# Performance work log

Measured on AMD Instinct MI355X. Metric: run time of the kernel, lower is better.

## Reference

```python
import jax, jax.numpy as jnp
import numpy as np

SCALING = 2.0  # alpha / rank = 16 / 8


def _kron(A, B):
    # A: (m, n), B: (p, q) -> (m*p, n*q), same broadcast-multiply-reshape as torch code
    m, n = A.shape
    p, q = B.shape
    return (A[:, None, :, None] * B[None, :, None, :]).reshape(m * p, n * q)


def setup_inputs() -> dict:
    key = jax.random.key(0)
    k1, k2, k3, k4 = jax.random.split(key, 4)
    x = jax.random.normal(k1, (128, 8192), dtype=jnp.float32)
    original_weight = jax.random.normal(k2, (8192, 8192), dtype=jnp.float32) * 0.02
    lokr_A = jax.random.normal(k3, (512, 8192), dtype=jnp.float32) * 0.02
    lokr_B = jax.random.normal(k4, (16, 1), dtype=jnp.float32) * 0.02
    scalar = jnp.ones((1,), dtype=jnp.float32)
    return {"x": x, "original_weight": original_weight, "lokr_A": lokr_A,
            "lokr_B": lokr_B, "scalar": scalar}


def reference(x, original_weight, lokr_A, lokr_B, scalar):
    # delta_W = (A kron B) * scaling ; W_eff = W + scalar * delta_W ; out = x @ W_eff^T
    delta_W = _kron(lokr_A, lokr_B) * SCALING          # (8192, 8192)
    W_eff = original_weight + scalar[0] * delta_W      # bypass_mode with original weight
    return x @ W_eff.T                                 # dropout=0 -> identity
```

## Files before the change

### kernel.cpp

```cpp
#include <hip/hip_runtime.h>


#define M_DIM 128
#define N_DIM 8192
#define K_DIM 8192
#define BN 32
#define NWAVE 8
#define KW (K_DIM / NWAVE)

typedef __attribute__((ext_vector_type(8))) short bf16x8;
typedef __attribute__((ext_vector_type(4))) float f32x4;

__device__ __forceinline__ unsigned short f2bf(float f) {
  unsigned u = __builtin_bit_cast(unsigned, f);
  u += 0x7FFFu + ((u >> 16) & 1u);
  return (unsigned short)(u >> 16);
}

__device__ __forceinline__ bf16x8 cvt8(float4 a, float4 b) {
  bf16x8 r;
  r[0] = (short)f2bf(a.x); r[1] = (short)f2bf(a.y);
  r[2] = (short)f2bf(a.z); r[3] = (short)f2bf(a.w);
  r[4] = (short)f2bf(b.x); r[5] = (short)f2bf(b.y);
  r[6] = (short)f2bf(b.z); r[7] = (short)f2bf(b.w);
  return r;
}

__global__ void convert_x_kernel(const float4* __restrict__ x4,
                                 ushort4* __restrict__ xb4) {
  int t = blockIdx.x * blockDim.x + threadIdx.x;
  const int n4 = M_DIM * K_DIM / 4;
  for (int i = t; i < n4; i += gridDim.x * blockDim.x) {
    float4 v = x4[i];
    ushort4 o;
    o.x = f2bf(v.x); o.y = f2bf(v.y); o.z = f2bf(v.z); o.w = f2bf(v.w);
    xb4[i] = o;
  }
}

__global__ __launch_bounds__(512, 2) void lokr_main(
    const float* __restrict__ W,
    const float* __restrict__ A,
    const float* __restrict__ Bv,
    const float* __restrict__ scal,
    const unsigned short* __restrict__ xb,
    float* __restrict__ out)
{
  __shared__ float red[NWAVE * M_DIM * 16];

  const int t    = threadIdx.x;
  const int lane = t & 63;
  const int wv   = t >> 6;
  const int b    = blockIdx.x;
  const int l15  = lane & 15;
  const int l4   = lane >> 4;
  const int kw   = wv * KW;

  const float sB = 2.0f * scal[0] * Bv[l15];

  f32x4 accW[8][2];
  f32x4 accY[8];
  const f32x4 z4 = {0.f, 0.f, 0.f, 0.f};
#pragma unroll
  for (int mf = 0; mf < 8; ++mf) {
    accY[mf] = z4;
    accW[mf][0] = z4;
    accW[mf][1] = z4;
  }

  const float* Wp = W + (size_t)(b * BN + l15) * K_DIM + kw + l4 * 8;
  const float* Ap = A + (size_t)(2 * b + (l15 >> 3)) * K_DIM + kw + l4 * 8;
  const unsigned short* xp = xb + (size_t)l15 * K_DIM + kw + l4 * 8;

  float4 wr[2][2][2];
  float4 ar[2][2];
#pragma unroll
  for (int nf = 0; nf < 2; ++nf)
#pragma unroll
    for (int kk = 0; kk < 2; ++kk)
#pragma unroll
      for (int h = 0; h < 2; ++h)
        wr[nf][kk][h] = *(const float4*)(Wp + (size_t)nf * 16 * K_DIM + kk * 32 + h * 4);
#pragma unroll
  for (int kk = 0; kk < 2; ++kk)
#pragma unroll
    for (int h = 0; h < 2; ++h)
      ar[kk][h] = *(const float4*)(Ap + kk * 32 + h * 4);

  for (int kt = 0; kt < KW; kt += 64) {
    bf16x8 wbf[2][2], abf[2];
#pragma unroll
    for (int nf = 0; nf < 2; ++nf)
#pragma unroll
      for (int kk = 0; kk < 2; ++kk)
        wbf[nf][kk] = cvt8(wr[nf][kk][0], wr[nf][kk][1]);
#pragma unroll
    for (int kk = 0; kk < 2; ++kk)
      abf[kk] = cvt8(ar[kk][0], ar[kk][1]);

    if (kt + 64 < KW) {
#pragma unroll
      for (int nf = 0; nf < 2; ++nf)
#pragma unroll
        for (int kk = 0; kk < 2; ++kk)
#pragma unroll
          for (int h = 0; h < 2; ++h)
            wr[nf][kk][h] = *(const float4*)(Wp + (size_t)nf * 16 * K_DIM + kt + 64 + kk * 32 + h * 4);
#pragma unroll
      for (int kk = 0; kk < 2; ++kk)
#pragma unroll
        for (int h = 0; h < 2; ++h)
          ar[kk][h] = *(const float4*)(Ap + kt + 64 + kk * 32 + h * 4);
    }

#pragma unroll
    for (int kk = 0; kk < 2; ++kk) {
      bf16x8 xa[8];
#pragma unroll
      for (int mf = 0; mf < 8; ++mf)
        xa[mf] = *(const bf16x8*)(xp + (size_t)mf * 16 * K_DIM + kt + kk * 32);
#pragma unroll
      for (int mf = 0; mf < 8; ++mf) {
        accW[mf][0] = __builtin_amdgcn_mfma_f32_16x16x32_bf16(xa[mf], wbf[0][kk], accW[mf][0], 0, 0, 0);
        accW[mf][1] = __builtin_amdgcn_mfma_f32_16x16x32_bf16(xa[mf], wbf[1][kk], accW[mf][1], 0, 0, 0);
        accY[mf]    = __builtin_amdgcn_mfma_f32_16x16x32_bf16(xa[mf], abf[kk],    accY[mf],    0, 0, 0);
      }
    }
  }

#pragma unroll 1
  for (int nf = 0; nf < 2; ++nf) {
    if (nf) __syncthreads();
#pragma unroll
    for (int mf = 0; mf < 8; ++mf) {
#pragma unroll
      for (int r = 0; r < 4; ++r) {
        float y2v = __shfl(accY[mf][r], (lane & 48) | (nf << 3), 64);
        int m = mf * 16 + l4 * 4 + r;
        red[wv * 2048 + m * 16 + l15] = accW[mf][nf][r] + sB * y2v;
      }
    }
    __syncthreads();
    const float* rp = red + t * 4;
    float4 s = *(const float4*)rp;
#pragma unroll
    for (int w = 1; w < NWAVE; ++w) {
      float4 v = *(const float4*)(rp + w * 2048);
      s.x += v.x; s.y += v.y; s.z += v.z; s.w += v.w;
    }
    int m  = t >> 2;
    int c0 = (t & 3) * 4;
    *(float4*)(out + (size_t)m * N_DIM + b * BN + nf * 16 + c0) = s;
  }
}

extern "C" void kernel_launch(void* const* d_in, const int* in_sizes, int n_in,
                              void* d_out, int out_size, void* d_ws, size_t ws_size,
                              hipStream_t stream) {
  const float* x    = (const float*)d_in[0];
  const float* W    = (const float*)d_in[1];
  const float* A    = (const float*)d_in[2];
  const float* Bv   = (const float*)d_in[3];
  const float* scal = (const float*)d_in[4];
  float* out = (float*)d_out;

  unsigned short* xb = (unsigned short*)d_ws;

  convert_x_kernel<<<512, 256, 0, stream>>>((const float4*)x, (ushort4*)xb);
  lokr_main<<<N_DIM / BN, 512, 0, stream>>>(W, A, Bv, scal, xb, out);
}
```

Baseline: 454.5 us.

## Split waves across M and K halves with double-buffered W and x loads

Reorganizes the 8 waves into 2 M-groups by 4 K-slices, so each wave computes 64 rows over a 2048-wide K range with half the accumulators. Adds explicit ping-pong register buffering of W, A and the bf16 x fragments to overlap global loads with MFMA work. This reduces register pressure and x-load volume per wave, but each W/A element is now loaded and converted by two waves, increasing cache traffic and conversion ALU work.

```diff
diff --git a/kernel.cpp b/kernel.cpp
--- a/kernel.cpp
+++ b/kernel.cpp
@@ -5,8 +5,7 @@
 #define N_DIM 8192
 #define K_DIM 8192
 #define BN 32
-#define NWAVE 8
-#define KW (K_DIM / NWAVE)
+#define KWC (K_DIM / 4)
 
 typedef __attribute__((ext_vector_type(8))) short bf16x8;
 typedef __attribute__((ext_vector_type(4))) float f32x4;
@@ -38,6 +37,37 @@
   }
 }
 
+#define LOADW(koff, w, a) { \
+    w[0] = *(const float4*)(Wp + (koff)); \
+    w[1] = *(const float4*)(Wp + (koff) + 4); \
+    w[2] = *(const float4*)(Wp + 16 * (size_t)K_DIM + (koff)); \
+    w[3] = *(const float4*)(Wp + 16 * (size_t)K_DIM + (koff) + 4); \
+    a[0] = *(const float4*)(Ap + (koff)); \
+    a[1] = *(const float4*)(Ap + (koff) + 4); \
+  }
+
+#define LOADX(koff, x) { \
+    x[0] = *(const bf16x8*)(xp + (koff)); \
+    x[1] = *(const bf16x8*)(xp + 16 * (size_t)K_DIM + (koff)); \
+    x[2] = *(const bf16x8*)(xp + 32 * (size_t)K_DIM + (koff)); \
+    x[3] = *(const bf16x8*)(xp + 48 * (size_t)K_DIM + (koff)); \
+  }
+
+#define MFMA_STEP(x, w0, w1, ab) { \
+    accW[0][0] = __builtin_amdgcn_mfma_f32_16x16x32_bf16(x[0], w0, accW[0][0], 0, 0, 0); \
+    accW[0][1] = __builtin_amdgcn_mfma_f32_16x16x32_bf16(x[0], w1, accW[0][1], 0, 0, 0); \
+    accY[0]    = __builtin_amdgcn_mfma_f32_16x16x32_bf16(x[0], ab, accY[0],    0, 0, 0); \
+    accW[1][0] = __builtin_amdgcn_mfma_f32_16x16x32_bf16(x[1], w0, accW[1][0], 0, 0, 0); \
+    accW[1][1] = __builtin_amdgcn_mfma_f32_16x16x32_bf16(x[1], w1, accW[1][1], 0, 0, 0); \
+    accY[1]    = __builtin_amdgcn_mfma_f32_16x16x32_bf16(x[1], ab, accY[1],    0, 0, 0); \
+    accW[2][0] = __builtin_amdgcn_mfma_f32_16x16x32_bf16(x[2], w0, accW[2][0], 0, 0, 0); \
+    accW[2][1] = __builtin_amdgcn_mfma_f32_16x16x32_bf16(x[2], w1, accW[2][1], 0, 0, 0); \
+    accY[2]    = __builtin_amdgcn_mfma_f32_16x16x32_bf16(x[2], ab, accY[2],    0, 0, 0); \
+    accW[3][0] = __builtin_amdgcn_mfma_f32_16x16x32_bf16(x[3], w0, accW[3][0], 0, 0, 0); \
+    accW[3][1] = __builtin_amdgcn_mfma_f32_16x16x32_bf16(x[3], w1, accW[3][1], 0, 0, 0); \
+    accY[3]    = __builtin_amdgcn_mfma_f32_16x16x32_bf16(x[3], ab, accY[3],    0, 0, 0); \
+  }
+
 __global__ __launch_bounds__(512, 2) void lokr_main(
     const float* __restrict__ W,
     const float* __restrict__ A,
@@ -46,23 +76,25 @@
     const unsigned short* __restrict__ xb,
     float* __restrict__ out)
 {
-  __shared__ float red[NWAVE * M_DIM * 16];
+  __shared__ float red[8 * 64 * 16];
 
   const int t    = threadIdx.x;
   const int lane = t & 63;
   const int wv   = t >> 6;
+  const int kwi  = wv & 3;
+  const int mw   = wv >> 2;
   const int b    = blockIdx.x;
   const int l15  = lane & 15;
   const int l4   = lane >> 4;
-  const int kw   = wv * KW;
+  const int kw   = kwi * KWC;
 
   const float sB = 2.0f * scal[0] * Bv[l15];
 
-  f32x4 accW[8][2];
-  f32x4 accY[8];
+  f32x4 accW[4][2];
+  f32x4 accY[4];
   const f32x4 z4 = {0.f, 0.f, 0.f, 0.f};
 #pragma unroll
-  for (int mf = 0; mf < 8; ++mf) {
+  for (int mf = 0; mf < 4; ++mf) {
     accY[mf] = z4;
     accW[mf][0] = z4;
     accW[mf][1] = z4;
@@ -70,86 +102,57 @@
 
   const float* Wp = W + (size_t)(b * BN + l15) * K_DIM + kw + l4 * 8;
   const float* Ap = A + (size_t)(2 * b + (l15 >> 3)) * K_DIM + kw + l4 * 8;
-  const unsigned short* xp = xb + (size_t)l15 * K_DIM + kw + l4 * 8;
+  const unsigned short* xp = xb + (size_t)(mw * 64 + l15) * K_DIM + kw + l4 * 8;
 
-  float4 wr[2][2][2];
-  float4 ar[2][2];
-#pragma unroll
-  for (int nf = 0; nf < 2; ++nf)
-#pragma unroll
-    for (int kk = 0; kk < 2; ++kk)
-#pragma unroll
-      for (int h = 0; h < 2; ++h)
-        wr[nf][kk][h] = *(const float4*)(Wp + (size_t)nf * 16 * K_DIM + kk * 32 + h * 4);
-#pragma unroll
-  for (int kk = 0; kk < 2; ++kk)
-#pragma unroll
-    for (int h = 0; h < 2; ++h)
-      ar[kk][h] = *(const float4*)(Ap + kk * 32 + h * 4);
+  float4 wc[4], ac[2];
+  float4 wn[4], an[2];
+  bf16x8 xc[4], xn[4];
 
-  for (int kt = 0; kt < KW; kt += 64) {
-    bf16x8 wbf[2][2], abf[2];
-#pragma unroll
-    for (int nf = 0; nf < 2; ++nf)
-#pragma unroll
-      for (int kk = 0; kk < 2; ++kk)
-        wbf[nf][kk] = cvt8(wr[nf][kk][0], wr[nf][kk][1]);
-#pragma unroll
-    for (int kk = 0; kk < 2; ++kk)
-      abf[kk] = cvt8(ar[kk][0], ar[kk][1]);
+  LOADW(0, wc, ac);
+  LOADX(0, xc);
 
-    if (kt + 64 < KW) {
-#pragma unroll
-      for (int nf = 0; nf < 2; ++nf)
-#pragma unroll
-        for (int kk = 0; kk < 2; ++kk)
-#pragma unroll
-          for (int h = 0; h < 2; ++h)
-            wr[nf][kk][h] = *(const float4*)(Wp + (size_t)nf * 16 * K_DIM + kt + 64 + kk * 32 + h * 4);
-#pragma unroll
-      for (int kk = 0; kk < 2; ++kk)
-#pragma unroll
-        for (int h = 0; h < 2; ++h)
-          ar[kk][h] = *(const float4*)(Ap + kt + 64 + kk * 32 + h * 4);
+  for (int k = 0; k < KWC; k += 64) {
+    LOADW(k + 32, wn, an);
+    {
+      bf16x8 w0 = cvt8(wc[0], wc[1]);
+      bf16x8 w1 = cvt8(wc[2], wc[3]);
+      bf16x8 ab = cvt8(ac[0], ac[1]);
+      LOADX(k + 32, xn);
+      MFMA_STEP(xc, w0, w1, ab);
     }
-
-#pragma unroll
-    for (int kk = 0; kk < 2; ++kk) {
-      bf16x8 xa[8];
-#pragma unroll
-      for (int mf = 0; mf < 8; ++mf)
-        xa[mf] = *(const bf16x8*)(xp + (size_t)mf * 16 * K_DIM + kt + kk * 32);
-#pragma unroll
-      for (int mf = 0; mf < 8; ++mf) {
-        accW[mf][0] = __builtin_amdgcn_mfma_f32_16x16x32_bf16(xa[mf], wbf[0][kk], accW[mf][0], 0, 0, 0);
-        accW[mf][1] = __builtin_amdgcn_mfma_f32_16x16x32_bf16(xa[mf], wbf[1][kk], accW[mf][1], 0, 0, 0);
-        accY[mf]    = __builtin_amdgcn_mfma_f32_16x16x32_bf16(xa[mf], abf[kk],    accY[mf],    0, 0, 0);
-      }
+    if (k + 64 < KWC) LOADW(k + 64, wc, ac);
+    {
+      bf16x8 w0 = cvt8(wn[0], wn[1]);
+      bf16x8 w1 = cvt8(wn[2], wn[3]);
+      bf16x8 ab = cvt8(an[0], an[1]);
+      LOADX(k + 64, xc);
+      MFMA_STEP(xn, w0, w1, ab);
     }
   }
 
+  float* redp = red + wv * 1024;
 #pragma unroll 1
   for (int nf = 0; nf < 2; ++nf) {
     if (nf) __syncthreads();
 #pragma unroll
-    for (int mf = 0; mf < 8; ++mf) {
+    for (int mf = 0; mf < 4; ++mf) {
 #pragma unroll
       for (int r = 0; r < 4; ++r) {
         float y2v = __shfl(accY[mf][r], (lane & 48) | (nf << 3), 64);
-        int m = mf * 16 + l4 * 4 + r;
-        red[wv * 2048 + m * 16 + l15] = accW[mf][nf][r] + sB * y2v;
+        int mrel = mf * 16 + l4 * 4 + r;
+        redp[mrel * 16 + l15] = accW[mf][nf][r] + sB * y2v;
       }
     }
     __syncthreads();
-    const float* rp = red + t * 4;
+    int m  = t >> 2;
+    int c0 = (t & 3) * 4;
+    const float* rp = red + (m >> 6) * 4096 + (m & 63) * 16 + c0;
     float4 s = *(const float4*)rp;
 #pragma unroll
-    for (int w = 1; w < NWAVE; ++w) {
-      float4 v = *(const float4*)(rp + w * 2048);
+    for (int kp = 1; kp < 4; ++kp) {
+      float4 v = *(const float4*)(rp + kp * 1024);
       s.x += v.x; s.y += v.y; s.z += v.z; s.w += v.w;
     }
-    int m  = t >> 2;
-    int c0 = (t & 3) * 4;
     *(float4*)(out + (size_t)m * N_DIM + b * BN + nf * 16 + c0) = s;
   }
 }
```

Result: faster. 445.5 us (-2.0%).

## Split M across waves with LDS-staged x and shared bf16 W tiles

Applied to the files above, without the earlier changes.

Each wave previously owned a K slice and all 128 rows, with a cross-wave LDS reduction at the end. Now each of the 8 waves owns 16 rows of M over the full K. The x tile is streamed into a double-buffered, XOR-swizzled LDS buffer with global_load_lds. The W and A tiles are converted to bf16 once per block, stored in LDS and shared by all waves, which removes the final reduction and the large register accumulator arrays. The trade-off is a __syncthreads on every 64-wide K step and a longer serial K loop per wave, which may expose memory latency with only a two-step W prefetch.

```diff
diff --git a/kernel.cpp b/kernel.cpp
--- a/kernel.cpp
+++ b/kernel.cpp
@@ -5,8 +5,8 @@
 #define N_DIM 8192
 #define K_DIM 8192
 #define BN 32
-#define NWAVE 8
-#define KW (K_DIM / NWAVE)
+#define BK 64
+#define NSTEP (K_DIM / BK)
 
 typedef __attribute__((ext_vector_type(8))) short bf16x8;
 typedef __attribute__((ext_vector_type(4))) float f32x4;
@@ -15,15 +15,6 @@
   unsigned u = __builtin_bit_cast(unsigned, f);
   u += 0x7FFFu + ((u >> 16) & 1u);
   return (unsigned short)(u >> 16);
-}
-
-__device__ __forceinline__ bf16x8 cvt8(float4 a, float4 b) {
-  bf16x8 r;
-  r[0] = (short)f2bf(a.x); r[1] = (short)f2bf(a.y);
-  r[2] = (short)f2bf(a.z); r[3] = (short)f2bf(a.w);
-  r[4] = (short)f2bf(b.x); r[5] = (short)f2bf(b.y);
-  r[6] = (short)f2bf(b.z); r[7] = (short)f2bf(b.w);
-  return r;
 }
 
 __global__ void convert_x_kernel(const float4* __restrict__ x4,
@@ -38,7 +29,40 @@
   }
 }
 
-__global__ __launch_bounds__(512, 2) void lokr_main(
+#define GLDS2(KOFF, BUF) { \
+    __builtin_amdgcn_global_load_lds( \
+        (const __attribute__((address_space(1))) unsigned int*)(xs0 + (KOFF)), \
+        (__attribute__((address_space(3))) unsigned int*)(&xls[BUF][wv * 1024]), 16, 0, 0); \
+    __builtin_amdgcn_global_load_lds( \
+        (const __attribute__((address_space(1))) unsigned int*)(xs1 + (KOFF)), \
+        (__attribute__((address_space(3))) unsigned int*)(&xls[BUF][wv * 1024 + 512]), 16, 0, 0); \
+  }
+
+#define ITER(S, BF, WREG, AREG) { \
+    { ushort4 o; o.x = f2bf(WREG.x); o.y = f2bf(WREG.y); \
+      o.z = f2bf(WREG.z); o.w = f2bf(WREG.w); \
+      *(ushort4*)&wls[BF][t >> 4][(t & 15) * 4] = o; } \
+    if (aact) { ushort2 o2; o2.x = f2bf(AREG.x); o2.y = f2bf(AREG.y); \
+      *(ushort2*)&wls[BF][32 + (t >> 5)][(t & 31) * 2] = o2; } \
+    __syncthreads();   \
+    { int kn = ((S) + 2 < NSTEP ? (S) + 2 : NSTEP - 1) * BK; \
+      WREG = *(const float4*)(Wp + kn); \
+      if (aact) AREG = *(const float2*)(Apt + kn); } \
+    { int kx = ((S) + 1 < NSTEP ? (S) + 1 : NSTEP - 1) * BK; \
+      GLDS2(kx, (BF) ^ 1); } \
+    _Pragma("unroll") \
+    for (int kk = 0; kk < 2; ++kk) { \
+      bf16x8 xf = *(const bf16x8*)&xls[BF][(wv * 16 + l15) * BK + (((kk * 4 + l4) ^ (l15 & 7)) * 8)]; \
+      bf16x8 w0 = *(const bf16x8*)&wls[BF][l15][kk * 32 + l4 * 8]; \
+      bf16x8 w1 = *(const bf16x8*)&wls[BF][16 + l15][kk * 32 + l4 * 8]; \
+      bf16x8 af = *(const bf16x8*)&wls[BF][32 + (l15 >> 3)][kk * 32 + l4 * 8]; \
+      accW0 = __builtin_amdgcn_mfma_f32_16x16x32_bf16(xf, w0, accW0, 0, 0, 0); \
+      accW1 = __builtin_amdgcn_mfma_f32_16x16x32_bf16(xf, w1, accW1, 0, 0, 0); \
+      accY  = __builtin_amdgcn_mfma_f32_16x16x32_bf16(xf, af, accY, 0, 0, 0); \
+    } \
+  }
+
+__global__ __launch_bounds__(512) void lokr_main(
     const float* __restrict__ W,
     const float* __restrict__ A,
     const float* __restrict__ Bv,
@@ -46,7 +70,8 @@
     const unsigned short* __restrict__ xb,
     float* __restrict__ out)
 {
-  __shared__ float red[NWAVE * M_DIM * 16];
+  __shared__ unsigned short xls[2][M_DIM * BK];
+  __shared__ unsigned short wls[2][34][72];
 
   const int t    = threadIdx.x;
   const int lane = t & 63;
@@ -54,103 +79,43 @@
   const int b    = blockIdx.x;
   const int l15  = lane & 15;
   const int l4   = lane >> 4;
-  const int kw   = wv * KW;
 
   const float sB = 2.0f * scal[0] * Bv[l15];
 
-  f32x4 accW[8][2];
-  f32x4 accY[8];
-  const f32x4 z4 = {0.f, 0.f, 0.f, 0.f};
-#pragma unroll
-  for (int mf = 0; mf < 8; ++mf) {
-    accY[mf] = z4;
-    accW[mf][0] = z4;
-    accW[mf][1] = z4;
+  const float* Wp  = W + (size_t)(b * BN + (t >> 4)) * K_DIM + (t & 15) * 4;
+  const bool  aact = (t < 64);
+  const float* Apt = A + (size_t)(2 * b + ((t >> 5) & 1)) * K_DIM + (t & 31) * 2;
+
+  const int xr0 = wv * 16 + (lane >> 3);
+  const int xr1 = xr0 + 8;
+  const int xc  = lane & 7;
+  const unsigned short* xs0 = xb + (size_t)xr0 * K_DIM + ((xc ^ (xr0 & 7)) * 8);
+  const unsigned short* xs1 = xb + (size_t)xr1 * K_DIM + ((xc ^ (xr1 & 7)) * 8);
+
+  f32x4 accW0 = {0.f, 0.f, 0.f, 0.f};
+  f32x4 accW1 = {0.f, 0.f, 0.f, 0.f};
+  f32x4 accY  = {0.f, 0.f, 0.f, 0.f};
+
+  float4 wA = *(const float4*)(Wp);
+  float4 wB = *(const float4*)(Wp + BK);
+  float2 aA = {0.f, 0.f}, aB = {0.f, 0.f};
+  if (aact) { aA = *(const float2*)(Apt); aB = *(const float2*)(Apt + BK); }
+  GLDS2(0, 0);
+
+  for (int s2 = 0; s2 < NSTEP; s2 += 2) {
+    ITER(s2,     0, wA, aA);
+    ITER(s2 + 1, 1, wB, aB);
   }
 
-  const float* Wp = W + (size_t)(b * BN + l15) * K_DIM + kw + l4 * 8;
-  const float* Ap = A + (size_t)(2 * b + (l15 >> 3)) * K_DIM + kw + l4 * 8;
-  const unsigned short* xp = xb + (size_t)l15 * K_DIM + kw + l4 * 8;
-
-  float4 wr[2][2][2];
-  float4 ar[2][2];
+  const size_t ob = (size_t)(wv * 16 + l4 * 4) * N_DIM + (size_t)b * BN + l15;
 #pragma unroll
-  for (int nf = 0; nf < 2; ++nf)
+  for (int nf = 0; nf < 2; ++nf) {
+    f32x4 aw = nf ? accW1 : accW0;
 #pragma unroll
-    for (int kk = 0; kk < 2; ++kk)
-#pragma unroll
-      for (int h = 0; h < 2; ++h)
-        wr[nf][kk][h] = *(const float4*)(Wp + (size_t)nf * 16 * K_DIM + kk * 32 + h * 4);
-#pragma unroll
-  for (int kk = 0; kk < 2; ++kk)
-#pragma unroll
-    for (int h = 0; h < 2; ++h)
-      ar[kk][h] = *(const float4*)(Ap + kk * 32 + h * 4);
-
-  for (int kt = 0; kt < KW; kt += 64) {
-    bf16x8 wbf[2][2], abf[2];
-#pragma unroll
-    for (int nf = 0; nf < 2; ++nf)
-#pragma unroll
-      for (int kk = 0; kk < 2; ++kk)
-        wbf[nf][kk] = cvt8(wr[nf][kk][0], wr[nf][kk][1]);
-#pragma unroll
-    for (int kk = 0; kk < 2; ++kk)
-      abf[kk] = cvt8(ar[kk][0], ar[kk][1]);
-
-    if (kt + 64 < KW) {
-#pragma unroll
-      for (int nf = 0; nf < 2; ++nf)
-#pragma unroll
-        for (int kk = 0; kk < 2; ++kk)
-#pragma unroll
-          for (int h = 0; h < 2; ++h)
-            wr[nf][kk][h] = *(const float4*)(Wp + (size_t)nf * 16 * K_DIM + kt + 64 + kk * 32 + h * 4);
-#pragma unroll
-      for (int kk = 0; kk < 2; ++kk)
-#pragma unroll
-        for (int h = 0; h < 2; ++h)
-          ar[kk][h] = *(const float4*)(Ap + kt + 64 + kk * 32 + h * 4);
+    for (int r = 0; r < 4; ++r) {
+      float y2v = __shfl(accY[r], (lane & 48) | (nf << 3), 64);
+      out[ob + (size_t)r * N_DIM + nf * 16] = aw[r] + sB * y2v;
     }
-
-#pragma unroll
-    for (int kk = 0; kk < 2; ++kk) {
-      bf16x8 xa[8];
-#pragma unroll
-      for (int mf = 0; mf < 8; ++mf)
-        xa[mf] = *(const bf16x8*)(xp + (size_t)mf * 16 * K_DIM + kt + kk * 32);
-#pragma unroll
-      for (int mf = 0; mf < 8; ++mf) {
-        accW[mf][0] = __builtin_amdgcn_mfma_f32_16x16x32_bf16(xa[mf], wbf[0][kk], accW[mf][0], 0, 0, 0);
-        accW[mf][1] = __builtin_amdgcn_mfma_f32_16x16x32_bf16(xa[mf], wbf[1][kk], accW[mf][1], 0, 0, 0);
-        accY[mf]    = __builtin_amdgcn_mfma_f32_16x16x32_bf16(xa[mf], abf[kk],    accY[mf],    0, 0, 0);
-      }
-    }
-  }
-
-#pragma unroll 1
-  for (int nf = 0; nf < 2; ++nf) {
-    if (nf) __syncthreads();
-#pragma unroll
-    for (int mf = 0; mf < 8; ++mf) {
-#pragma unroll
-      for (int r = 0; r < 4; ++r) {
-        float y2v = __shfl(accY[mf][r], (lane & 48) | (nf << 3), 64);
-        int m = mf * 16 + l4 * 4 + r;
-        red[wv * 2048 + m * 16 + l15] = accW[mf][nf][r] + sB * y2v;
-      }
-    }
-    __syncthreads();
-    const float* rp = red + t * 4;
-    float4 s = *(const float4*)rp;
-#pragma unroll
-    for (int w = 1; w < NWAVE; ++w) {
-      float4 v = *(const float4*)(rp + w * 2048);
-      s.x += v.x; s.y += v.y; s.z += v.z; s.w += v.w;
-    }
-    int m  = t >> 2;
-    int c0 = (t & 3) * 4;
-    *(float4*)(out + (size_t)m * N_DIM + b * BN + nf * 16 + c0) = s;
   }
 }
 
```

Measured after the change: 448.7 us. Within noise of the previous version (-1.3%).
